# Optimization experiments

Hardware: AMD Instinct MI355X
Metric: run time of the kernel (lower is better)

Reference implementation:

```python
import jax, jax.numpy as jnp
import numpy as np

OMEGA = 10.0
SIGMA = 10.0
HID = 256
IN_DIM = 3
OUT_DIM = 3


def gabor(x, W, b):
    # torch.nn.Linear: lin = x @ W.T + b
    lin = x @ W.T + b
    # exp(1j*omega*lin - (sigma*lin)**2).real == cos(omega*lin) * exp(-(sigma*lin)**2)
    return jnp.cos(OMEGA * lin) * jnp.exp(-jnp.square(SIGMA * lin))


def _linear_init(key, out_dim, in_dim):
    kw, kb = jax.random.split(key)
    bound = 1.0 / np.sqrt(in_dim)
    W = jax.random.uniform(kw, (out_dim, in_dim), jnp.float32, -bound, bound)
    b = jax.random.uniform(kb, (out_dim,), jnp.float32, -bound, bound)
    return W, b


def setup_inputs() -> dict:
    key = jax.random.key(0)
    keys = jax.random.split(key, 7)
    N = 262144
    x = jax.random.uniform(keys[0], (N, IN_DIM), jnp.float32)
    W0, b0 = _linear_init(keys[1], HID, IN_DIM)
    W1, b1 = _linear_init(keys[2], HID, HID)
    W2, b2 = _linear_init(keys[3], HID, HID)
    W3, b3 = _linear_init(keys[4], HID, HID + IN_DIM)  # skip-concat layer
    W4, b4 = _linear_init(keys[5], HID, HID)
    Wf, bf = _linear_init(keys[6], OUT_DIM, HID)
    return {"x": x, "W0": W0, "b0": b0, "W1": W1, "b1": b1, "W2": W2,
            "b2": b2, "W3": W3, "b3": b3, "W4": W4, "b4": b4,
            "Wf": Wf, "bf": bf}


def reference(x, W0, b0, W1, b1, W2, b2, W3, b3, W4, b4, Wf, bf):
    x_in = x
    h = gabor(x, W0, b0)          # net[0]
    h = gabor(h, W1, b1)          # net[1]
    h = gabor(h, W2, b2)          # net[2]
    h = jnp.concatenate([h, x_in], axis=-1)  # skip before net[3]
    h = gabor(h, W3, b3)          # net[3]
    h = gabor(h, W4, b4)          # net[4]
    return h @ Wf.T + bf          # final linear
```

## Files before the change

### kernel.cpp

```cpp
#include <hip/hip_runtime.h>

typedef _Float16 f16x8 __attribute__((ext_vector_type(8)));
typedef _Float16 f16x4 __attribute__((ext_vector_type(4)));
typedef float    f32x4 __attribute__((ext_vector_type(4)));

#define BN    64
#define KPAD  288
#define ROWB  (KPAD * 2)
#define WELE  270336

__device__ __forceinline__ int swz(int row, int colb) {
  int c = (colb < 512) ? (colb ^ ((row & 7) << 4)) : colb;
  return row * ROWB + c;
}

__device__ __forceinline__ float gabor_f(float lin) {
  float a = 10.f * lin;
  return __cosf(a) * __expf(-a * a);
}

template <int KS>
__device__ __forceinline__ void mfma_layer(const char* __restrict__ inb,
                                           char* __restrict__ outb,
                                           const _Float16* __restrict__ Wh,
                                           const _Float16* __restrict__ Wl,
                                           const float* __restrict__ bias,
                                           int lane, int wid, int phase) {
  const int r = lane & 15;
  const int g = lane >> 4;
  const int n0 = wid * 32;
  f32x4 acc[2][4];
#pragma unroll
  for (int i = 0; i < 2; i++)
#pragma unroll
    for (int j = 0; j < 4; j++) {
      f32x4 z = {0.f, 0.f, 0.f, 0.f};
      acc[i][j] = z;
    }

#pragma unroll
  for (int kk = 0; kk < KS; kk++) {
    int kkr = kk + phase;
    if (kkr >= KS) kkr -= KS;

    const int wof = (wid * KS + kkr) * 1024 + lane * 8;
    f16x8 a0 = *(const f16x8*)(Wh + wof);
    f16x8 a1 = *(const f16x8*)(Wh + wof + 512);
    f16x8 c0 = *(const f16x8*)(Wl + wof);
    f16x8 c1 = *(const f16x8*)(Wl + wof + 512);

    const int kb = kkr * 32 + g * 8;
    f16x8 b0 = *(const f16x8*)(inb + swz(0 * 16 + r, kb * 2));
    f16x8 b1 = *(const f16x8*)(inb + swz(1 * 16 + r, kb * 2));
    f16x8 b2 = *(const f16x8*)(inb + swz(2 * 16 + r, kb * 2));
    f16x8 b3 = *(const f16x8*)(inb + swz(3 * 16 + r, kb * 2));

    acc[0][0] = __builtin_amdgcn_mfma_f32_16x16x32_f16(a0, b0, acc[0][0], 0, 0, 0);
    acc[0][1] = __builtin_amdgcn_mfma_f32_16x16x32_f16(a0, b1, acc[0][1], 0, 0, 0);
    acc[0][2] = __builtin_amdgcn_mfma_f32_16x16x32_f16(a0, b2, acc[0][2], 0, 0, 0);
    acc[0][3] = __builtin_amdgcn_mfma_f32_16x16x32_f16(a0, b3, acc[0][3], 0, 0, 0);
    acc[1][0] = __builtin_amdgcn_mfma_f32_16x16x32_f16(a1, b0, acc[1][0], 0, 0, 0);
    acc[1][1] = __builtin_amdgcn_mfma_f32_16x16x32_f16(a1, b1, acc[1][1], 0, 0, 0);
    acc[1][2] = __builtin_amdgcn_mfma_f32_16x16x32_f16(a1, b2, acc[1][2], 0, 0, 0);
    acc[1][3] = __builtin_amdgcn_mfma_f32_16x16x32_f16(a1, b3, acc[1][3], 0, 0, 0);
    acc[0][0] = __builtin_amdgcn_mfma_f32_16x16x32_f16(c0, b0, acc[0][0], 0, 0, 0);
    acc[0][1] = __builtin_amdgcn_mfma_f32_16x16x32_f16(c0, b1, acc[0][1], 0, 0, 0);
    acc[0][2] = __builtin_amdgcn_mfma_f32_16x16x32_f16(c0, b2, acc[0][2], 0, 0, 0);
    acc[0][3] = __builtin_amdgcn_mfma_f32_16x16x32_f16(c0, b3, acc[0][3], 0, 0, 0);
    acc[1][0] = __builtin_amdgcn_mfma_f32_16x16x32_f16(c1, b0, acc[1][0], 0, 0, 0);
    acc[1][1] = __builtin_amdgcn_mfma_f32_16x16x32_f16(c1, b1, acc[1][1], 0, 0, 0);
    acc[1][2] = __builtin_amdgcn_mfma_f32_16x16x32_f16(c1, b2, acc[1][2], 0, 0, 0);
    acc[1][3] = __builtin_amdgcn_mfma_f32_16x16x32_f16(c1, b3, acc[1][3], 0, 0, 0);
  }

#pragma unroll
  for (int i = 0; i < 2; i++) {
    const f32x4 bv = *(const f32x4*)(bias + n0 + i * 16 + g * 4);
#pragma unroll
    for (int j = 0; j < 4; j++) {
      f16x4 hv;
#pragma unroll
      for (int e = 0; e < 4; e++)
        hv[e] = (_Float16)gabor_f(acc[i][j][e] + bv[e]);
      *(f16x4*)(outb + swz(j * 16 + r, (n0 + i * 16 + g * 4) * 2)) = hv;
    }
  }
}

extern "C" __global__ void __launch_bounds__(512, 4)
inr_fused(const float* __restrict__ x, const float* __restrict__ W0,
          const float* __restrict__ b0, const float* __restrict__ b1,
          const float* __restrict__ b2, const float* __restrict__ b3,
          const float* __restrict__ b4, const float* __restrict__ Wf,
          const float* __restrict__ bf, const _Float16* __restrict__ wsh,
          float* __restrict__ out, int npts) {
  extern __shared__ char smem[];
  char* bufA = smem;
  char* bufB = smem + BN * ROWB;

  const _Float16* w1h = wsh;
  const _Float16* w2h = wsh + 65536;
  const _Float16* w4h = wsh + 131072;
  const _Float16* w3p = wsh + 196608;
  const _Float16* w1l = wsh + WELE;
  const _Float16* w2l = wsh + WELE + 65536;
  const _Float16* w4l = wsh + WELE + 131072;
  const _Float16* w3l = wsh + WELE + 196608;

  const int tid   = threadIdx.x;
  const int pbase = blockIdx.x * BN;
  const int phase = blockIdx.x & 7;

  {
    const int p = tid >> 3;
    const int q = tid & 7;
    const int gp = pbase + p;
    float x0 = 0.f, x1 = 0.f, x2 = 0.f;
    if (gp < npts) {
      x0 = x[(size_t)gp * 3 + 0];
      x1 = x[(size_t)gp * 3 + 1];
      x2 = x[(size_t)gp * 3 + 2];
    }
#pragma unroll
    for (int ub = 0; ub < 32; ub += 8) {
      const int u0 = q * 32 + ub;
      f16x8 hv;
#pragma unroll
      for (int e = 0; e < 8; e++) {
        const int u = u0 + e;
        float lin = fmaf(x0, W0[u * 3 + 0],
                    fmaf(x1, W0[u * 3 + 1],
                    fmaf(x2, W0[u * 3 + 2], b0[u])));
        hv[e] = (_Float16)gabor_f(lin);
      }
      *(f16x8*)(bufA + swz(p, u0 * 2)) = hv;
    }
    if (q < 4) {
      f16x8 xv = {(_Float16)0.f, (_Float16)0.f, (_Float16)0.f, (_Float16)0.f,
                  (_Float16)0.f, (_Float16)0.f, (_Float16)0.f, (_Float16)0.f};
      if (q == 0) { xv[0] = (_Float16)x0; xv[1] = (_Float16)x1; xv[2] = (_Float16)x2; }
      *(f16x8*)(bufA + swz(p, (256 + q * 8) * 2)) = xv;
    }
  }
  __syncthreads();

  const int lane = tid & 63;
  const int wid  = tid >> 6;

  mfma_layer<8>(bufA, bufB, w1h, w1l, b1, lane, wid, phase);
  __syncthreads();
  mfma_layer<8>(bufB, bufA, w2h, w2l, b2, lane, wid, phase);
  __syncthreads();
  mfma_layer<9>(bufA, bufB, w3p, w3l, b3, lane, wid, phase);
  __syncthreads();
  mfma_layer<8>(bufB, bufA, w4h, w4l, b4, lane, wid, phase);
  __syncthreads();

  if (tid < BN * 3) {
    const int p = tid / 3;
    const int o = tid - p * 3;
    const int gp = pbase + p;
    if (gp < npts) {
      float a0 = bf[o], a1 = 0.f, a2 = 0.f, a3 = 0.f;
#pragma unroll 4
      for (int k = 0; k < 256; k += 8) {
        f16x8 hv = *(const f16x8*)(bufA + swz(p, k * 2));
        f32x4 wa = *(const f32x4*)(Wf + o * 256 + k);
        f32x4 wb = *(const f32x4*)(Wf + o * 256 + k + 4);
        a0 = fmaf((float)hv[0], wa[0], a0);
        a1 = fmaf((float)hv[1], wa[1], a1);
        a2 = fmaf((float)hv[2], wa[2], a2);
        a3 = fmaf((float)hv[3], wa[3], a3);
        a0 = fmaf((float)hv[4], wb[0], a0);
        a1 = fmaf((float)hv[5], wb[1], a1);
        a2 = fmaf((float)hv[6], wb[2], a2);
        a3 = fmaf((float)hv[7], wb[3], a3);
      }
      out[(size_t)gp * 3 + o] = (a0 + a1) + (a2 + a3);
    }
  }
}

extern "C" __global__ void conv_w(const float* __restrict__ W1,
                                  const float* __restrict__ W2,
                                  const float* __restrict__ W4,
                                  const float* __restrict__ W3,
                                  _Float16* __restrict__ wsh) {
  int idx = blockIdx.x * blockDim.x + threadIdx.x;
  if (idx >= WELE) return;

  int base, KS;
  const float* src = nullptr;
  int ldk = 256, kmax = 256;
  if (idx < 65536)       { base = 0;      KS = 8; src = W1; }
  else if (idx < 131072) { base = 65536;  KS = 8; src = W2; }
  else if (idx < 196608) { base = 131072; KS = 8; src = W4; }
  else                   { base = 196608; KS = 9; src = W3; ldk = 259; kmax = 259; }

  const int t    = idx - base;
  const int e    = t & 7;
  const int lane = (t >> 3) & 63;
  const int i    = (t >> 9) & 1;
  const int rem  = t >> 10;
  const int kk   = rem % KS;
  const int slice = rem / KS;

  const int unit = slice * 32 + i * 16 + (lane & 15);
  const int k    = kk * 32 + (lane >> 4) * 8 + e;

  const float w = (k < kmax) ? src[(size_t)unit * ldk + k] : 0.f;
  const _Float16 hi = (_Float16)w;
  const _Float16 lo = (_Float16)(w - (float)hi);
  wsh[idx] = hi;
  wsh[idx + WELE] = lo;
}

extern "C" void kernel_launch(void* const* d_in, const int* in_sizes, int n_in,
                              void* d_out, int out_size, void* d_ws, size_t ws_size,
                              hipStream_t stream) {
  const float* x  = (const float*)d_in[0];
  const float* W0 = (const float*)d_in[1];
  const float* b0 = (const float*)d_in[2];
  const float* W1 = (const float*)d_in[3];
  const float* b1 = (const float*)d_in[4];
  const float* W2 = (const float*)d_in[5];
  const float* b2 = (const float*)d_in[6];
  const float* W3 = (const float*)d_in[7];
  const float* b3 = (const float*)d_in[8];
  const float* W4 = (const float*)d_in[9];
  const float* b4 = (const float*)d_in[10];
  const float* Wf = (const float*)d_in[11];
  const float* bf = (const float*)d_in[12];
  float* out      = (float*)d_out;
  _Float16* wsh   = (_Float16*)d_ws;

  const int npts = in_sizes[0] / 3;

  conv_w<<<(WELE + 511) / 512, 512, 0, stream>>>(W1, W2, W4, W3, wsh);

  const int nblk = (npts + BN - 1) / BN;
  inr_fused<<<nblk, 512, 2 * BN * ROWB, stream>>>(x, W0, b0, b1, b2, b3, b4,
                                                  Wf, bf, wsh, out, npts);
}
```

Measured before the change: 401.3 us.

## Software-pipeline MFMA operand loads with register double buffering and sched barriers

Each MFMA layer now prefetches the next k-step's weight fragments from global memory and activation fragments from LDS into a second register set while the current 16 MFMAs run. sched_group_barrier hints ask the compiler to interleave the loads with the MFMA group. Layer biases are also staged once into extra LDS at kernel start instead of being read from global per layer. The double buffering raises VGPR pressure, which under launch_bounds(512,4) could cause spills, and the extra 4 KB of LDS may reduce occupancy.

New measurement: 427.7 us. 6.6% more time.

```diff
diff --git a/kernel.cpp b/kernel.cpp
--- a/kernel.cpp
+++ b/kernel.cpp
@@ -8,6 +8,13 @@
 #define KPAD  288
 #define ROWB  (KPAD * 2)
 #define WELE  270336
+#define LDS_ACT (2 * BN * ROWB)
+#define LDS_TOTAL (LDS_ACT + 4096)
+
+#define SGB(mask, n) __builtin_amdgcn_sched_group_barrier((mask), (n), 0)
+#define SG_MFMA   0x8
+#define SG_VMEM_R 0x20
+#define SG_DS_R   0x100
 
 __device__ __forceinline__ int swz(int row, int colb) {
   int c = (colb < 512) ? (colb ^ ((row & 7) << 4)) : colb;
@@ -24,7 +31,7 @@
                                            char* __restrict__ outb,
                                            const _Float16* __restrict__ Wh,
                                            const _Float16* __restrict__ Wl,
-                                           const float* __restrict__ bias,
+                                           const float* __restrict__ lbias,
                                            int lane, int wid, int phase) {
   const int r = lane & 15;
   const int g = lane >> 4;
@@ -38,44 +45,69 @@
       acc[i][j] = z;
     }
 
+  f16x8 a0[2], a1[2], c0[2], c1[2], b[2][4];
+
+  {
+    const int kkr = (phase >= KS) ? 0 + 0 : phase;
+    const int wof = (wid * KS + kkr) * 1024 + lane * 8;
+    a0[0] = *(const f16x8*)(Wh + wof);
+    a1[0] = *(const f16x8*)(Wh + wof + 512);
+    c0[0] = *(const f16x8*)(Wl + wof);
+    c1[0] = *(const f16x8*)(Wl + wof + 512);
+    const int kb = kkr * 32 + g * 8;
+#pragma unroll
+    for (int j = 0; j < 4; j++)
+      b[0][j] = *(const f16x8*)(inb + swz(j * 16 + r, kb * 2));
+    SGB(SG_VMEM_R, 4);
+    SGB(SG_DS_R, 4);
+  }
+
 #pragma unroll
   for (int kk = 0; kk < KS; kk++) {
-    int kkr = kk + phase;
-    if (kkr >= KS) kkr -= KS;
-
-    const int wof = (wid * KS + kkr) * 1024 + lane * 8;
-    f16x8 a0 = *(const f16x8*)(Wh + wof);
-    f16x8 a1 = *(const f16x8*)(Wh + wof + 512);
-    f16x8 c0 = *(const f16x8*)(Wl + wof);
-    f16x8 c1 = *(const f16x8*)(Wl + wof + 512);
-
-    const int kb = kkr * 32 + g * 8;
-    f16x8 b0 = *(const f16x8*)(inb + swz(0 * 16 + r, kb * 2));
-    f16x8 b1 = *(const f16x8*)(inb + swz(1 * 16 + r, kb * 2));
-    f16x8 b2 = *(const f16x8*)(inb + swz(2 * 16 + r, kb * 2));
-    f16x8 b3 = *(const f16x8*)(inb + swz(3 * 16 + r, kb * 2));
-
-    acc[0][0] = __builtin_amdgcn_mfma_f32_16x16x32_f16(a0, b0, acc[0][0], 0, 0, 0);
-    acc[0][1] = __builtin_amdgcn_mfma_f32_16x16x32_f16(a0, b1, acc[0][1], 0, 0, 0);
-    acc[0][2] = __builtin_amdgcn_mfma_f32_16x16x32_f16(a0, b2, acc[0][2], 0, 0, 0);
-    acc[0][3] = __builtin_amdgcn_mfma_f32_16x16x32_f16(a0, b3, acc[0][3], 0, 0, 0);
-    acc[1][0] = __builtin_amdgcn_mfma_f32_16x16x32_f16(a1, b0, acc[1][0], 0, 0, 0);
-    acc[1][1] = __builtin_amdgcn_mfma_f32_16x16x32_f16(a1, b1, acc[1][1], 0, 0, 0);
-    acc[1][2] = __builtin_amdgcn_mfma_f32_16x16x32_f16(a1, b2, acc[1][2], 0, 0, 0);
-    acc[1][3] = __builtin_amdgcn_mfma_f32_16x16x32_f16(a1, b3, acc[1][3], 0, 0, 0);
-    acc[0][0] = __builtin_amdgcn_mfma_f32_16x16x32_f16(c0, b0, acc[0][0], 0, 0, 0);
-    acc[0][1] = __builtin_amdgcn_mfma_f32_16x16x32_f16(c0, b1, acc[0][1], 0, 0, 0);
-    acc[0][2] = __builtin_amdgcn_mfma_f32_16x16x32_f16(c0, b2, acc[0][2], 0, 0, 0);
-    acc[0][3] = __builtin_amdgcn_mfma_f32_16x16x32_f16(c0, b3, acc[0][3], 0, 0, 0);
-    acc[1][0] = __builtin_amdgcn_mfma_f32_16x16x32_f16(c1, b0, acc[1][0], 0, 0, 0);
-    acc[1][1] = __builtin_amdgcn_mfma_f32_16x16x32_f16(c1, b1, acc[1][1], 0, 0, 0);
-    acc[1][2] = __builtin_amdgcn_mfma_f32_16x16x32_f16(c1, b2, acc[1][2], 0, 0, 0);
-    acc[1][3] = __builtin_amdgcn_mfma_f32_16x16x32_f16(c1, b3, acc[1][3], 0, 0, 0);
+    const int cur = kk & 1;
+    const int nxt = cur ^ 1;
+
+    if (kk + 1 < KS) {
+      int kkr = kk + 1 + phase;
+      if (kkr >= KS) kkr -= KS;
+      const int wof = (wid * KS + kkr) * 1024 + lane * 8;
+      a0[nxt] = *(const f16x8*)(Wh + wof);
+      a1[nxt] = *(const f16x8*)(Wh + wof + 512);
+      c0[nxt] = *(const f16x8*)(Wl + wof);
+      c1[nxt] = *(const f16x8*)(Wl + wof + 512);
+      const int kb = kkr * 32 + g * 8;
+#pragma unroll
+      for (int j = 0; j < 4; j++)
+        b[nxt][j] = *(const f16x8*)(inb + swz(j * 16 + r, kb * 2));
+    }
+
+    acc[0][0] = __builtin_amdgcn_mfma_f32_16x16x32_f16(a0[cur], b[cur][0], acc[0][0], 0, 0, 0);
+    acc[0][1] = __builtin_amdgcn_mfma_f32_16x16x32_f16(a0[cur], b[cur][1], acc[0][1], 0, 0, 0);
+    acc[0][2] = __builtin_amdgcn_mfma_f32_16x16x32_f16(a0[cur], b[cur][2], acc[0][2], 0, 0, 0);
+    acc[0][3] = __builtin_amdgcn_mfma_f32_16x16x32_f16(a0[cur], b[cur][3], acc[0][3], 0, 0, 0);
+    acc[1][0] = __builtin_amdgcn_mfma_f32_16x16x32_f16(a1[cur], b[cur][0], acc[1][0], 0, 0, 0);
+    acc[1][1] = __builtin_amdgcn_mfma_f32_16x16x32_f16(a1[cur], b[cur][1], acc[1][1], 0, 0, 0);
+    acc[1][2] = __builtin_amdgcn_mfma_f32_16x16x32_f16(a1[cur], b[cur][2], acc[1][2], 0, 0, 0);
+    acc[1][3] = __builtin_amdgcn_mfma_f32_16x16x32_f16(a1[cur], b[cur][3], acc[1][3], 0, 0, 0);
+    acc[0][0] = __builtin_amdgcn_mfma_f32_16x16x32_f16(c0[cur], b[cur][0], acc[0][0], 0, 0, 0);
+    acc[0][1] = __builtin_amdgcn_mfma_f32_16x16x32_f16(c0[cur], b[cur][1], acc[0][1], 0, 0, 0);
+    acc[0][2] = __builtin_amdgcn_mfma_f32_16x16x32_f16(c0[cur], b[cur][2], acc[0][2], 0, 0, 0);
+    acc[0][3] = __builtin_amdgcn_mfma_f32_16x16x32_f16(c0[cur], b[cur][3], acc[0][3], 0, 0, 0);
+    acc[1][0] = __builtin_amdgcn_mfma_f32_16x16x32_f16(c1[cur], b[cur][0], acc[1][0], 0, 0, 0);
+    acc[1][1] = __builtin_amdgcn_mfma_f32_16x16x32_f16(c1[cur], b[cur][1], acc[1][1], 0, 0, 0);
+    acc[1][2] = __builtin_amdgcn_mfma_f32_16x16x32_f16(c1[cur], b[cur][2], acc[1][2], 0, 0, 0);
+    acc[1][3] = __builtin_amdgcn_mfma_f32_16x16x32_f16(c1[cur], b[cur][3], acc[1][3], 0, 0, 0);
+
+    if (kk + 1 < KS) {
+      SGB(SG_VMEM_R, 4);
+      SGB(SG_DS_R, 4);
+    }
+    SGB(SG_MFMA, 16);
   }
 
 #pragma unroll
   for (int i = 0; i < 2; i++) {
-    const f32x4 bv = *(const f32x4*)(bias + n0 + i * 16 + g * 4);
+    const f32x4 bv = *(const f32x4*)(lbias + n0 + i * 16 + g * 4);
 #pragma unroll
     for (int j = 0; j < 4; j++) {
       f16x4 hv;
@@ -97,6 +129,7 @@
   extern __shared__ char smem[];
   char* bufA = smem;
   char* bufB = smem + BN * ROWB;
+  float* lbias = (float*)(smem + LDS_ACT);
 
   const _Float16* w1h = wsh;
   const _Float16* w2h = wsh + 65536;
@@ -110,6 +143,13 @@
   const int tid   = threadIdx.x;
   const int pbase = blockIdx.x * BN;
   const int phase = blockIdx.x & 7;
+
+  if (tid < 256) {
+    lbias[tid]       = b1[tid];
+    lbias[256 + tid] = b2[tid];
+    lbias[512 + tid] = b3[tid];
+    lbias[768 + tid] = b4[tid];
+  }
 
   {
     const int p = tid >> 3;
@@ -147,13 +187,14 @@
   const int lane = tid & 63;
   const int wid  = tid >> 6;
 
-  mfma_layer<8>(bufA, bufB, w1h, w1l, b1, lane, wid, phase);
-  __syncthreads();
-  mfma_layer<8>(bufB, bufA, w2h, w2l, b2, lane, wid, phase);
-  __syncthreads();
-  mfma_layer<9>(bufA, bufB, w3p, w3l, b3, lane, wid, phase);
-  __syncthreads();
-  mfma_layer<8>(bufB, bufA, w4h, w4l, b4, lane, wid, phase);
+  mfma_layer<8>(bufA, bufB, w1h, w1l, lbias,       lane, wid, phase);
+  __syncthreads();
+  mfma_layer<8>(bufB, bufA, w2h, w2l, lbias + 256, lane, wid, phase);
+  __syncthreads();
+  mfma_layer<9>(bufA, bufB, w3p, w3l, lbias + 512, lane, wid,
+                phase > 8 ? 8 : phase);
+  __syncthreads();
+  mfma_layer<8>(bufB, bufA, w4h, w4l, lbias + 768, lane, wid, phase);
   __syncthreads();
 
   if (tid < BN * 3) {
@@ -239,6 +280,6 @@
   conv_w<<<(WELE + 511) / 512, 512, 0, stream>>>(W1, W2, W4, W3, wsh);
 
   const int nblk = (npts + BN - 1) / BN;
-  inr_fused<<<nblk, 512, 2 * BN * ROWB, stream>>>(x, W0, b0, b1, b2, b3, b4,
-                                                  Wf, bf, wsh, out, npts);
-}
+  inr_fused<<<nblk, 512, LDS_TOTAL, stream>>>(x, W0, b0, b1, b2, b3, b4,
+                                              Wf, bf, wsh, out, npts);
+}
```

## Shrink point tile to 48 and use asymmetric LDS row strides

Applied to the files above, without the earlier changes.

Reduces points per block from 64 to 48, so each warp computes three 16-point column tiles instead of four. The buffer that only ever holds 256-wide activations uses a 512-byte row stride instead of 576, which trims shared memory per block. Launch bounds drop from 4 to 3 blocks per CU, and there are more blocks in total. The aim is to lower register and LDS pressure and spread the work over more blocks. The cost is that each weight fragment loaded from global memory feeds fewer MFMAs, so weight traffic per point rises.

After: 440.3 us. 1.1x slower.

```diff
diff --git a/kernel.cpp b/kernel.cpp
--- a/kernel.cpp
+++ b/kernel.cpp
@@ -4,14 +4,15 @@
 typedef _Float16 f16x4 __attribute__((ext_vector_type(4)));
 typedef float    f32x4 __attribute__((ext_vector_type(4)));
 
-#define BN    64
-#define KPAD  288
-#define ROWB  (KPAD * 2)
+#define BN    48
+#define ROWA  576
+#define ROWB2 512
 #define WELE  270336
-
-__device__ __forceinline__ int swz(int row, int colb) {
+#define LDS_TOTAL (BN * ROWA + BN * ROWB2)
+
+__device__ __forceinline__ int swzr(int row, int colb, int rb) {
   int c = (colb < 512) ? (colb ^ ((row & 7) << 4)) : colb;
-  return row * ROWB + c;
+  return row * rb + c;
 }
 
 __device__ __forceinline__ float gabor_f(float lin) {
@@ -19,7 +20,7 @@
   return __cosf(a) * __expf(-a * a);
 }
 
-template <int KS>
+template <int KS, int RIN, int ROUT>
 __device__ __forceinline__ void mfma_layer(const char* __restrict__ inb,
                                            char* __restrict__ outb,
                                            const _Float16* __restrict__ Wh,
@@ -29,11 +30,11 @@
   const int r = lane & 15;
   const int g = lane >> 4;
   const int n0 = wid * 32;
-  f32x4 acc[2][4];
+  f32x4 acc[2][3];
 #pragma unroll
   for (int i = 0; i < 2; i++)
 #pragma unroll
-    for (int j = 0; j < 4; j++) {
+    for (int j = 0; j < 3; j++) {
       f32x4 z = {0.f, 0.f, 0.f, 0.f};
       acc[i][j] = z;
     }
@@ -50,44 +51,39 @@
     f16x8 c1 = *(const f16x8*)(Wl + wof + 512);
 
     const int kb = kkr * 32 + g * 8;
-    f16x8 b0 = *(const f16x8*)(inb + swz(0 * 16 + r, kb * 2));
-    f16x8 b1 = *(const f16x8*)(inb + swz(1 * 16 + r, kb * 2));
-    f16x8 b2 = *(const f16x8*)(inb + swz(2 * 16 + r, kb * 2));
-    f16x8 b3 = *(const f16x8*)(inb + swz(3 * 16 + r, kb * 2));
+    f16x8 b0 = *(const f16x8*)(inb + swzr(0 * 16 + r, kb * 2, RIN));
+    f16x8 b1 = *(const f16x8*)(inb + swzr(1 * 16 + r, kb * 2, RIN));
+    f16x8 b2 = *(const f16x8*)(inb + swzr(2 * 16 + r, kb * 2, RIN));
 
     acc[0][0] = __builtin_amdgcn_mfma_f32_16x16x32_f16(a0, b0, acc[0][0], 0, 0, 0);
     acc[0][1] = __builtin_amdgcn_mfma_f32_16x16x32_f16(a0, b1, acc[0][1], 0, 0, 0);
     acc[0][2] = __builtin_amdgcn_mfma_f32_16x16x32_f16(a0, b2, acc[0][2], 0, 0, 0);
-    acc[0][3] = __builtin_amdgcn_mfma_f32_16x16x32_f16(a0, b3, acc[0][3], 0, 0, 0);
     acc[1][0] = __builtin_amdgcn_mfma_f32_16x16x32_f16(a1, b0, acc[1][0], 0, 0, 0);
     acc[1][1] = __builtin_amdgcn_mfma_f32_16x16x32_f16(a1, b1, acc[1][1], 0, 0, 0);
     acc[1][2] = __builtin_amdgcn_mfma_f32_16x16x32_f16(a1, b2, acc[1][2], 0, 0, 0);
-    acc[1][3] = __builtin_amdgcn_mfma_f32_16x16x32_f16(a1, b3, acc[1][3], 0, 0, 0);
     acc[0][0] = __builtin_amdgcn_mfma_f32_16x16x32_f16(c0, b0, acc[0][0], 0, 0, 0);
     acc[0][1] = __builtin_amdgcn_mfma_f32_16x16x32_f16(c0, b1, acc[0][1], 0, 0, 0);
     acc[0][2] = __builtin_amdgcn_mfma_f32_16x16x32_f16(c0, b2, acc[0][2], 0, 0, 0);
-    acc[0][3] = __builtin_amdgcn_mfma_f32_16x16x32_f16(c0, b3, acc[0][3], 0, 0, 0);
     acc[1][0] = __builtin_amdgcn_mfma_f32_16x16x32_f16(c1, b0, acc[1][0], 0, 0, 0);
     acc[1][1] = __builtin_amdgcn_mfma_f32_16x16x32_f16(c1, b1, acc[1][1], 0, 0, 0);
     acc[1][2] = __builtin_amdgcn_mfma_f32_16x16x32_f16(c1, b2, acc[1][2], 0, 0, 0);
-    acc[1][3] = __builtin_amdgcn_mfma_f32_16x16x32_f16(c1, b3, acc[1][3], 0, 0, 0);
   }
 
 #pragma unroll
   for (int i = 0; i < 2; i++) {
     const f32x4 bv = *(const f32x4*)(bias + n0 + i * 16 + g * 4);
 #pragma unroll
-    for (int j = 0; j < 4; j++) {
+    for (int j = 0; j < 3; j++) {
       f16x4 hv;
 #pragma unroll
       for (int e = 0; e < 4; e++)
         hv[e] = (_Float16)gabor_f(acc[i][j][e] + bv[e]);
-      *(f16x4*)(outb + swz(j * 16 + r, (n0 + i * 16 + g * 4) * 2)) = hv;
-    }
-  }
-}
-
-extern "C" __global__ void __launch_bounds__(512, 4)
+      *(f16x4*)(outb + swzr(j * 16 + r, (n0 + i * 16 + g * 4) * 2, ROUT)) = hv;
+    }
+  }
+}
+
+extern "C" __global__ void __launch_bounds__(512, 3)
 inr_fused(const float* __restrict__ x, const float* __restrict__ W0,
           const float* __restrict__ b0, const float* __restrict__ b1,
           const float* __restrict__ b2, const float* __restrict__ b3,
@@ -96,7 +92,7 @@
           float* __restrict__ out, int npts) {
   extern __shared__ char smem[];
   char* bufA = smem;
-  char* bufB = smem + BN * ROWB;
+  char* bufB = smem + BN * ROWA;
 
   const _Float16* w1h = wsh;
   const _Float16* w2h = wsh + 65536;
@@ -114,32 +110,34 @@
   {
     const int p = tid >> 3;
     const int q = tid & 7;
-    const int gp = pbase + p;
-    float x0 = 0.f, x1 = 0.f, x2 = 0.f;
-    if (gp < npts) {
-      x0 = x[(size_t)gp * 3 + 0];
-      x1 = x[(size_t)gp * 3 + 1];
-      x2 = x[(size_t)gp * 3 + 2];
-    }
-#pragma unroll
-    for (int ub = 0; ub < 32; ub += 8) {
-      const int u0 = q * 32 + ub;
-      f16x8 hv;
-#pragma unroll
-      for (int e = 0; e < 8; e++) {
-        const int u = u0 + e;
-        float lin = fmaf(x0, W0[u * 3 + 0],
-                    fmaf(x1, W0[u * 3 + 1],
-                    fmaf(x2, W0[u * 3 + 2], b0[u])));
-        hv[e] = (_Float16)gabor_f(lin);
-      }
-      *(f16x8*)(bufA + swz(p, u0 * 2)) = hv;
-    }
-    if (q < 4) {
-      f16x8 xv = {(_Float16)0.f, (_Float16)0.f, (_Float16)0.f, (_Float16)0.f,
-                  (_Float16)0.f, (_Float16)0.f, (_Float16)0.f, (_Float16)0.f};
-      if (q == 0) { xv[0] = (_Float16)x0; xv[1] = (_Float16)x1; xv[2] = (_Float16)x2; }
-      *(f16x8*)(bufA + swz(p, (256 + q * 8) * 2)) = xv;
+    if (p < BN) {
+      const int gp = pbase + p;
+      float x0 = 0.f, x1 = 0.f, x2 = 0.f;
+      if (gp < npts) {
+        x0 = x[(size_t)gp * 3 + 0];
+        x1 = x[(size_t)gp * 3 + 1];
+        x2 = x[(size_t)gp * 3 + 2];
+      }
+#pragma unroll
+      for (int ub = 0; ub < 32; ub += 8) {
+        const int u0 = q * 32 + ub;
+        f16x8 hv;
+#pragma unroll
+        for (int e = 0; e < 8; e++) {
+          const int u = u0 + e;
+          float lin = fmaf(x0, W0[u * 3 + 0],
+                      fmaf(x1, W0[u * 3 + 1],
+                      fmaf(x2, W0[u * 3 + 2], b0[u])));
+          hv[e] = (_Float16)gabor_f(lin);
+        }
+        *(f16x8*)(bufA + swzr(p, u0 * 2, ROWA)) = hv;
+      }
+      if (q < 4) {
+        f16x8 xv = {(_Float16)0.f, (_Float16)0.f, (_Float16)0.f, (_Float16)0.f,
+                    (_Float16)0.f, (_Float16)0.f, (_Float16)0.f, (_Float16)0.f};
+        if (q == 0) { xv[0] = (_Float16)x0; xv[1] = (_Float16)x1; xv[2] = (_Float16)x2; }
+        *(f16x8*)(bufA + swzr(p, (256 + q * 8) * 2, ROWA)) = xv;
+      }
     }
   }
   __syncthreads();
@@ -147,13 +145,13 @@
   const int lane = tid & 63;
   const int wid  = tid >> 6;
 
-  mfma_layer<8>(bufA, bufB, w1h, w1l, b1, lane, wid, phase);
-  __syncthreads();
-  mfma_layer<8>(bufB, bufA, w2h, w2l, b2, lane, wid, phase);
-  __syncthreads();
-  mfma_layer<9>(bufA, bufB, w3p, w3l, b3, lane, wid, phase);
-  __syncthreads();
-  mfma_layer<8>(bufB, bufA, w4h, w4l, b4, lane, wid, phase);
+  mfma_layer<8, ROWA, ROWB2>(bufA, bufB, w1h, w1l, b1, lane, wid, phase);
+  __syncthreads();
+  mfma_layer<8, ROWB2, ROWA>(bufB, bufA, w2h, w2l, b2, lane, wid, phase);
+  __syncthreads();
+  mfma_layer<9, ROWA, ROWB2>(bufA, bufB, w3p, w3l, b3, lane, wid, phase);
+  __syncthreads();
+  mfma_layer<8, ROWB2, ROWA>(bufB, bufA, w4h, w4l, b4, lane, wid, phase);
   __syncthreads();
 
   if (tid < BN * 3) {
@@ -164,7 +162,7 @@
       float a0 = bf[o], a1 = 0.f, a2 = 0.f, a3 = 0.f;
 #pragma unroll 4
       for (int k = 0; k < 256; k += 8) {
-        f16x8 hv = *(const f16x8*)(bufA + swz(p, k * 2));
+        f16x8 hv = *(const f16x8*)(bufA + swzr(p, k * 2, ROWA));
         f32x4 wa = *(const f32x4*)(Wf + o * 256 + k);
         f32x4 wb = *(const f32x4*)(Wf + o * 256 + k + 4);
         a0 = fmaf((float)hv[0], wa[0], a0);
@@ -239,6 +237,6 @@
   conv_w<<<(WELE + 511) / 512, 512, 0, stream>>>(W1, W2, W4, W3, wsh);
 
   const int nblk = (npts + BN - 1) / BN;
-  inr_fused<<<nblk, 512, 2 * BN * ROWB, stream>>>(x, W0, b0, b1, b2, b3, b4,
-                                                  Wf, bf, wsh, out, npts);
-}
+  inr_fused<<<nblk, 512, LDS_TOTAL, stream>>>(x, W0, b0, b1, b2, b3, b4,
+                                              Wf, bf, wsh, out, npts);
+}
```
